# Optimization experiments

Hardware: AMD Instinct MI355X
Metric: run time of the kernel (lower is better)

Reference implementation:

```python
import jax, jax.numpy as jnp
import numpy as np

NBINS = (128, 64, 32)
LOG2PI = float(np.log(2.0 * np.pi))


def _quadratic_spline_stack(x, genes_oi, local_gene_ix, delta, uh, uw):
    """Stack of piecewise-quadratic (piecewise-linear density) splines on [0,1].
    Per split with n heights / n-1 widths (n-1 bins). Returns (outputs, logabsdet)."""
    uh_oi = uh[genes_oi]  # [G, sum(n)]
    uw_oi = uw[genes_oi]  # [G, sum(n-1)]
    outputs = x
    logabsdet = jnp.zeros_like(x)
    oh = ow = od = 0
    for n in NBINS:
        nh, nw = n, n - 1
        uhs = uh_oi[:, oh:oh + nh]
        uws = uw_oi[:, ow:ow + nw]
        ds = delta[:, od:od + nh]
        oh += nh; ow += nw; od += nh
        # per-gene bin widths / locations
        widths_g = jax.nn.softmax(uws, axis=-1)                     # [G, nw]
        bl = jnp.cumsum(widths_g, axis=-1)
        bl = bl.at[:, -1].set(1.0)
        bin_loc_g = jnp.pad(bl, ((0, 0), (1, 0)))                   # [G, nw+1]
        # gather per cut
        w = widths_g[local_gene_ix]                                 # [N, nw]
        loc = bin_loc_g[local_gene_ix]                              # [N, nw+1]
        # per-cut knot heights: gene baseline + cell/gene delta, normalized to unit area
        h_un = jnp.exp(uhs[local_gene_ix] + ds)                     # [N, nh]
        area = jnp.sum(0.5 * (h_un[:, :-1] + h_un[:, 1:]) * w, axis=-1, keepdims=True)
        h = h_un / area                                             # [N, nh]
        seg = 0.5 * (h[:, :-1] + h[:, 1:]) * w                      # bin masses [N, nw]
        left_cdf = jnp.pad(jnp.cumsum(seg, axis=-1)[:, :-1], ((0, 0), (1, 0)))  # [N, nw]
        # locate bin
        bin_idx = jnp.clip(jnp.sum(outputs[:, None] >= loc, axis=-1) - 1, 0, nw - 1)
        gi = bin_idx[:, None]
        loc_l = jnp.take_along_axis(loc, gi, -1)[:, 0]
        w_b = jnp.take_along_axis(w, gi, -1)[:, 0]
        cdf_l = jnp.take_along_axis(left_cdf, gi, -1)[:, 0]
        h_l = jnp.take_along_axis(h, gi, -1)[:, 0]
        h_r = jnp.take_along_axis(h, gi + 1, -1)[:, 0]
        alpha = (outputs - loc_l) / w_b
        outputs = (0.5 * (h_r - h_l) * w_b) * alpha * alpha + h_l * w_b * alpha + cdf_l
        logabsdet = logabsdet + jnp.log(h_l + (h_r - h_l) * alpha)
    return outputs, logabsdet


def setup_inputs() -> dict:
    key = jax.random.key(0)
    ks = jax.random.split(key, 10)
    B, L, G_total, G_oi, C, N = 512, 16, 20000, 500, 224, 200000
    clustering = jax.random.uniform(ks[0], (B, L), dtype=jnp.float32)
    coordinates = jax.random.uniform(ks[1], (N,), dtype=jnp.float32, minval=1e-4, maxval=1.0 - 1e-4)
    genes_oi = jax.random.randint(ks[2], (G_oi,), 0, G_total)
    local_gene_ix = jax.random.randint(ks[3], (N,), 0, G_oi)
    local_cellxgene_ix = jax.random.randint(ks[4], (N,), 0, B * G_oi)
    localcellxgene_ix = jax.random.randint(ks[5], (N,), 0, B * G_total)
    logit_weight = jax.random.normal(ks[6], (G_total, L, C), dtype=jnp.float32) * 0.01
    rho_weight = jax.random.normal(ks[7], (G_total, L), dtype=jnp.float32) * 0.05
    rho_bias = 1e-5 + (1.0 - 1e-5) * jax.random.uniform(ks[8], (G_total,), dtype=jnp.float32)
    k9, k10 = jax.random.split(ks[9])
    unnormalized_heights = jax.random.normal(k9, (G_total, sum(NBINS)), dtype=jnp.float32) * 0.1
    unnormalized_widths = jax.random.normal(k10, (G_total, sum(n - 1 for n in NBINS)), dtype=jnp.float32) * 0.1
    return dict(clustering=clustering, coordinates=coordinates, genes_oi=genes_oi,
                local_gene_ix=local_gene_ix, local_cellxgene_ix=local_cellxgene_ix,
                localcellxgene_ix=localcellxgene_ix, logit_weight=logit_weight,
                rho_weight=rho_weight, rho_bias=rho_bias,
                unnormalized_heights=unnormalized_heights,
                unnormalized_widths=unnormalized_widths)


def reference(clustering, coordinates, genes_oi, local_gene_ix, local_cellxgene_ix,
              localcellxgene_ix, logit_weight, rho_weight, rho_bias,
              unnormalized_heights, unnormalized_widths):
    B = clustering.shape[0]
    G = genes_oi.shape[0]
    n_total_genes = rho_bias.shape[0]
    # Decoder (n_layers=0 -> nn_output = latent)
    lw_oi = logit_weight[genes_oi]                                   # [G, L, C]
    mixture_delta = jnp.einsum('bl,glc->bgc', clustering, lw_oi)     # [B, G, C]
    rho_delta = clustering @ rho_weight.T                            # [B, G_total]
    rho = jax.nn.softmax(jnp.log(rho_bias)[None, :] + rho_delta, axis=-1)
    rho_cuts = rho.reshape(-1)[localcellxgene_ix]                    # [N]
    md_cuts = mixture_delta.reshape(B * G, -1)[local_cellxgene_ix]   # [N, C]
    _, lik_mixture = _quadratic_spline_stack(coordinates, genes_oi, local_gene_ix,
                                             md_cuts, unnormalized_heights, unnormalized_widths)
    lik_overall = jnp.log(rho_cuts) + jnp.log(jnp.float32(n_total_genes))
    elbo = -jnp.sum(lik_mixture + lik_overall)
    # Normal(0, exp(log_scale=0)=1) regularization log-probs
    def normal_logpdf(v):
        return -0.5 * v * v - 0.5 * LOG2PI
    elbo = elbo - jnp.sum(normal_logpdf(lw_oi))
    elbo = elbo - jnp.sum(normal_logpdf(rho_weight[genes_oi]))
    return elbo
```

## Files before the change

kernel.cpp:

```cpp
#include <hip/hip_runtime.h>
#include <cstddef>

#define LOG2PI_F 1.8378770664093453f

typedef float f2 __attribute__((ext_vector_type(2)));

__device__ __forceinline__ float wave_sum(float v) {
#pragma unroll
    for (int o = 32; o >= 1; o >>= 1) v += __shfl_xor(v, o, 64);
    return v;
}
__device__ __forceinline__ float wave_max(float v) {
#pragma unroll
    for (int o = 32; o >= 1; o >>= 1) v = fmaxf(v, __shfl_xor(v, o, 64));
    return v;
}
__device__ __forceinline__ float wave_scan_incl(float v, int lane) {
#pragma unroll
    for (int o = 1; o < 64; o <<= 1) {
        float t = __shfl_up(v, o, 64);
        if (lane >= o) v += t;
    }
    return v;
}

__device__ __forceinline__ float dot16(const f2* __restrict__ a, const f2* __restrict__ b) {
    f2 dv = a[0] * b[0];
#pragma unroll
    for (int l = 1; l < 8; ++l) dv = __builtin_elementwise_fma(a[l], b[l], dv);
    return dv.x + dv.y;
}

__global__ void k_prep_genes(const int* __restrict__ genes_oi,
                             const float* __restrict__ uh, const float* __restrict__ uw,
                             float4* __restrict__ pk, int* __restrict__ counts, int G_oi) {
    const int g = blockIdx.x;
    const int t = threadIdx.x;
    if (t == 0) counts[g] = 0;
    const int gs = genes_oi[g];
    const float* uhg = uh + (size_t)gs * 224;
    const float* uwg = uw + (size_t)gs * 221;

    const int NH[3] = {128, 64, 32};
    const int OH[3] = {0, 128, 192};
    const int OW[3] = {0, 127, 190};
    const int SO[3] = {0, 128, 191};
#pragma unroll
    for (int lev = 0; lev < 3; ++lev) {
        const int nw = NH[lev] - 1;
        float v0 = (t < nw)      ? uwg[OW[lev] + t]      : -INFINITY;
        float v1 = (t + 64 < nw) ? uwg[OW[lev] + t + 64] : -INFINITY;
        float mx = wave_max(fmaxf(v0, v1));
        float e0 = (t < nw)      ? __expf(v0 - mx) : 0.f;
        float e1 = (t + 64 < nw) ? __expf(v1 - mx) : 0.f;
        float inv = 1.0f / wave_sum(e0 + e1);
        float w0 = e0 * inv, w1 = e1 * inv;
        float i0 = wave_scan_incl(w0, t);
        float tot0 = __shfl(i0, 63, 64);
        float i1 = wave_scan_incl(w1, t) + tot0;
        if (t < nw) {
            float loc = (t == nw - 1) ? 1.0f : i0;
            pk[(size_t)(SO[lev] + t) * G_oi + g] = make_float4(uhg[OH[lev] + t + 1], 0.5f * w0, loc, 0.f);
        }
        if (t + 64 < nw) {
            int j = t + 64;
            float loc = (j == nw - 1) ? 1.0f : i1;
            pk[(size_t)(SO[lev] + j) * G_oi + g] = make_float4(uhg[OH[lev] + j + 1], 0.5f * w1, loc, 0.f);
        }
    }
    if (t == 0) pk[(size_t)127 * G_oi + g] = make_float4(uhg[0], uhg[128], uhg[192], 0.f);
}

__global__ void k_prep_lwT(const int* __restrict__ genes_oi,
                           const float* __restrict__ lw, const float* __restrict__ rw,
                           float* __restrict__ lwT, float* __restrict__ pB) {
    const int g = blockIdx.x;
    const int tid = threadIdx.x;
    const int gs = genes_oi[g];
    const float* src = lw + (size_t)gs * 3584;
    float* dst = lwT + (size_t)g * 3584;
    float acc = 0.f;
    if (tid < 224) {
        float vv[16];
#pragma unroll
        for (int l = 0; l < 16; ++l) {
            float v = src[l * 224 + tid];
            vv[l] = v;
            acc = fmaf(v, v, acc);
        }
        float4* d4 = (float4*)(dst + (size_t)tid * 16);
#pragma unroll
        for (int q = 0; q < 4; ++q)
            d4[q] = make_float4(vv[4 * q + 0], vv[4 * q + 1], vv[4 * q + 2], vv[4 * q + 3]);
    }
    if (tid < 16) { float v = rw[(size_t)gs * 16 + tid]; acc = fmaf(v, v, acc); }
    __shared__ float sm[256];
    sm[tid] = acc;
    __syncthreads();
    for (int o = 128; o > 0; o >>= 1) { if (tid < o) sm[tid] += sm[tid + o]; __syncthreads(); }
    if (tid == 0) pB[g] = 0.5f * sm[0] + 0.5f * LOG2PI_F * (3584.0f + 16.0f);
}

__global__ void k_hist_logrb(const int* __restrict__ lcx, int* __restrict__ counts,
                             const float* __restrict__ rho_bias, float* __restrict__ logrb,
                             int N, int G_oi, int G_total) {
    int i = blockIdx.x * blockDim.x + threadIdx.x;
    if (i < G_total) logrb[i] = __logf(rho_bias[i]);
    if (i < N) atomicAdd(&counts[(unsigned)lcx[i] % (unsigned)G_oi], 1);
}

__global__ void k_scan(const int* __restrict__ counts, int* __restrict__ offsets,
                       int* __restrict__ cursor, int G_oi) {
    __shared__ int sm[512];
    const int t = threadIdx.x;
    int v = (t < G_oi) ? counts[t] : 0;
    sm[t] = v;
    __syncthreads();
    for (int o = 1; o < 512; o <<= 1) {
        int add = (t >= o) ? sm[t - o] : 0;
        __syncthreads();
        sm[t] += add;
        __syncthreads();
    }
    if (t < G_oi) {
        offsets[t + 1] = sm[t];
        cursor[t] = sm[t] - v;
    }
    if (t == 0) offsets[0] = 0;
}

__global__ void k_scatter(const float* __restrict__ coord, const int* __restrict__ lgix,
                          const int* __restrict__ lcx, const int* __restrict__ lc2,
                          int* __restrict__ cursor, float4* __restrict__ xv, int N, int G_oi) {
    int i = blockIdx.x * blockDim.x + threadIdx.x;
    if (i >= N) return;
    unsigned v = (unsigned)lcx[i];
    unsigned g = v % (unsigned)G_oi;
    int pos = atomicAdd(&cursor[g], 1);
    int b1 = (int)(v / (unsigned)G_oi);
    xv[pos] = make_float4(coord[i], __int_as_float((b1 << 16) | lgix[i]),
                          __int_as_float(lc2[i]), 0.f);
}

__global__ void k_lse4(const float* __restrict__ clustering, const float* __restrict__ rw,
                       const float* __restrict__ logrb, float* __restrict__ lse,
                       int G_total, int B) {
    const int b0 = blockIdx.x * 4;
    const int tid = threadIdx.x;
    const int nc = min(4, B - b0);

    f2 cl[4][8];
#pragma unroll
    for (int c = 0; c < 4; ++c) {
        if (c < nc) {
            const float4* c4 = (const float4*)(clustering + (size_t)(b0 + c) * 16);
#pragma unroll
            for (int q = 0; q < 4; ++q) {
                float4 v = c4[q];
                cl[c][2 * q + 0] = (f2){v.x, v.y};
                cl[c][2 * q + 1] = (f2){v.z, v.w};
            }
        } else {
#pragma unroll
            for (int l = 0; l < 8; ++l) cl[c][l] = (f2){0.f, 0.f};
        }
    }

    float m[4], s[4];
#pragma unroll
    for (int c = 0; c < 4; ++c) { m[c] = -INFINITY; s[c] = 0.f; }

    for (int g = tid; g < G_total; g += 256) {
        const float4* r4 = (const float4*)(rw + (size_t)g * 16);
        f2 rv[8];
#pragma unroll
        for (int q = 0; q < 4; ++q) {
            float4 v = r4[q];
            rv[2 * q + 0] = (f2){v.x, v.y};
            rv[2 * q + 1] = (f2){v.z, v.w};
        }
        const float lb = logrb[g];
#pragma unroll
        for (int c = 0; c < 4; ++c) {
            float d = dot16(cl[c], rv);
            float logit = lb + d;
            float mn = fmaxf(m[c], logit);
            s[c] = s[c] * __expf(m[c] - mn) + __expf(logit - mn);
            m[c] = mn;
        }
    }

    __shared__ float ms[4][256], ss[4][256];
#pragma unroll
    for (int c = 0; c < 4; ++c) { ms[c][tid] = m[c]; ss[c][tid] = s[c]; }
    __syncthreads();
    for (int o = 128; o > 0; o >>= 1) {
        if (tid < o) {
#pragma unroll
            for (int c = 0; c < 4; ++c) {
                float m2 = ms[c][tid + o], s2 = ss[c][tid + o];
                float mn = fmaxf(ms[c][tid], m2);
                ss[c][tid] = ss[c][tid] * __expf(ms[c][tid] - mn) + s2 * __expf(m2 - mn);
                ms[c][tid] = mn;
            }
        }
        __syncthreads();
    }
    if (tid < 4 && tid < nc) lse[b0 + tid] = ms[tid][0] + __logf(ss[tid][0]);
}

__launch_bounds__(512, 4)
__global__ void k_main2(const float4* __restrict__ xv,
                        const int* __restrict__ offsets,
                        const float* __restrict__ clustering,
                        const float* __restrict__ lwT,
                        const float4* __restrict__ pk,
                        const float* __restrict__ rw,
                        const float* __restrict__ logrb,
                        const float* __restrict__ lse,
                        float* __restrict__ pA, int G_oi, int G_total) {
    const int g = blockIdx.x;
    const int tid = threadIdx.x;
    const float* lwg = lwT + (size_t)g * 3584;
    const int s = offsets[g], e = offsets[g + 1];
    const float logGt = __logf((float)G_total);
    float acc = 0.f;

    __shared__ int    s_cnt[512];
    __shared__ int    s_cur[512];
    __shared__ float4 s_v[512];
    __shared__ float  wsm[8];

    for (int base = s; base < e; base += 512) {
        const int cnt = min(512, e - base);
        const bool valid = tid < cnt;
        float4 v0 = xv[valid ? base + tid : s];
        const int gh_0 = __float_as_int(v0.y) & 0xffff;

        s_cnt[tid] = 0;
        __syncthreads();
        if (valid) atomicAdd(&s_cnt[gh_0], 1);
        __syncthreads();
        int v = s_cnt[tid];
        for (int o = 1; o < 512; o <<= 1) {
            int add = (tid >= o) ? s_cnt[tid - o] : 0;
            __syncthreads();
            s_cnt[tid] += add;
            __syncthreads();
        }
        s_cur[tid] = s_cnt[tid] - v;
        __syncthreads();
        if (valid) {
            int pos = atomicAdd(&s_cur[gh_0], 1);
            s_v[pos] = v0;
        }
        __syncthreads();

        if (valid) {
            float4 vv = s_v[tid];
            float x = vv.x;
            const int meta = __float_as_int(vv.y);
            const int gh  = meta & 0xffff;
            const int b1  = meta >> 16;
            const int lc2 = __float_as_int(vv.z);

            f2 cl[8];
            {
                const float4* c4 = (const float4*)(clustering + (size_t)b1 * 16);
#pragma unroll
                for (int q = 0; q < 4; ++q) {
                    float4 t4 = c4[q];
                    cl[2 * q + 0] = (f2){t4.x, t4.y};
                    cl[2 * q + 1] = (f2){t4.z, t4.w};
                }
            }
            const float4 uh0 = pk[(size_t)127 * G_oi + gh];
            const float uh0v[3] = {uh0.x, uh0.y, uh0.z};

            float lad = 0.f;
            const int NH[3] = {128, 64, 32};
            const int OH[3] = {0, 128, 192};
            const int SO[3] = {0, 128, 191};
#pragma unroll
            for (int lev = 0; lev < 3; ++lev) {
                const int nw = NH[lev] - 1;
                const float* rowbase = lwg + (size_t)OH[lev] * 16;
                float hp = __expf(uh0v[lev] + dot16((const f2*)rowbase, cl));
                float h_l = hp, h_r = hp, whb = 0.f, loc_l = 0.f, cdf = 0.f, area = 0.f;
                int in = 0;
                const float4* pks = pk + (size_t)SO[lev] * G_oi + gh;
                for (int j = 0; j < nw; ++j) {
                    const f2* row = (const f2*)(rowbase + (size_t)(j + 1) * 16);
                    float d = dot16(row, cl);
                    float4 pkv = *pks;
                    pks += G_oi;
                    float hn = __expf(pkv.x + d);
                    float seg = (hp + hn) * pkv.y;
                    bool inJ = (in == j);
                    if (inJ) { h_r = hn; whb = pkv.y; }
                    bool adv = (x >= pkv.z) && (j < nw - 1);
                    if (adv) { cdf += seg; h_l = hn; loc_l = pkv.z; in = j + 1; }
                    area += seg;
                    hp = hn;
                }
                float inv_area = __builtin_amdgcn_rcpf(area);
                float alpha = (x - loc_l) * 0.5f * __builtin_amdgcn_rcpf(whb);
                float t2 = whb * alpha;
                x = (t2 * fmaf(h_r - h_l, alpha, 2.f * h_l) + cdf) * inv_area;
                lad += __logf(fmaf(h_r - h_l, alpha, h_l)) - __logf(area);
            }

            unsigned b2 = (unsigned)lc2 / (unsigned)G_total;
            unsigned gt = (unsigned)lc2 - b2 * (unsigned)G_total;
            f2 c2[8], r2[8];
            {
                const float4* c24 = (const float4*)(clustering + (size_t)b2 * 16);
                const float4* r4  = (const float4*)(rw + (size_t)gt * 16);
#pragma unroll
                for (int q = 0; q < 4; ++q) {
                    float4 a = c24[q], b = r4[q];
                    c2[2 * q + 0] = (f2){a.x, a.y}; c2[2 * q + 1] = (f2){a.z, a.w};
                    r2[2 * q + 0] = (f2){b.x, b.y}; r2[2 * q + 1] = (f2){b.z, b.w};
                }
            }
            float d2 = dot16(c2, r2);
            float lik = logrb[gt] + d2 - lse[b2] + logGt;
            acc -= (lad + lik);
        }
    }

    acc = wave_sum(acc);
    if ((tid & 63) == 0) wsm[tid >> 6] = acc;
    __syncthreads();
    if (tid == 0) {
        float t = 0.f;
#pragma unroll
        for (int w = 0; w < 8; ++w) t += wsm[w];
        pA[g] = t;
    }
}

__global__ void k_final(const float* __restrict__ pA, const float* __restrict__ pB,
                        float* __restrict__ out, int nA, int nB) {
    const int tid = threadIdx.x;
    float acc = 0.f;
    for (int i = tid; i < nA; i += blockDim.x) acc += pA[i];
    for (int i = tid; i < nB; i += blockDim.x) acc += pB[i];
    __shared__ float sm[256];
    sm[tid] = acc;
    __syncthreads();
    for (int o = 128; o > 0; o >>= 1) { if (tid < o) sm[tid] += sm[tid + o]; __syncthreads(); }
    if (tid == 0) out[0] = sm[0];
}

extern "C" void kernel_launch(void* const* d_in, const int* in_sizes, int n_in,
                              void* d_out, int out_size, void* d_ws, size_t ws_size,
                              hipStream_t stream) {
    const float* clustering        = (const float*)d_in[0];
    const float* coordinates       = (const float*)d_in[1];
    const int*   genes_oi          = (const int*)d_in[2];
    const int*   local_gene_ix     = (const int*)d_in[3];
    const int*   local_cellxgene_ix= (const int*)d_in[4];
    const int*   localcellxgene_ix = (const int*)d_in[5];
    const float* lw                = (const float*)d_in[6];
    const float* rw                = (const float*)d_in[7];
    const float* rho_bias          = (const float*)d_in[8];
    const float* uh                = (const float*)d_in[9];
    const float* uw                = (const float*)d_in[10];

    const int G_total = in_sizes[8];
    const int G_oi    = in_sizes[2];
    const int N       = in_sizes[1];
    const int L       = in_sizes[7] / G_total;
    const int B       = in_sizes[0] / L;

    size_t off = 0;
    char* base = (char*)d_ws;
    auto alloc = [&](size_t nbytes) {
        char* p = base + off;
        off = (off + nbytes + 15) & ~(size_t)15;
        return (void*)p;
    };
    float*  pA      = (float*)alloc(sizeof(float) * (G_oi + 16));
    float*  pB      = (float*)alloc(sizeof(float) * (G_oi + 16));
    float*  lse     = (float*)alloc(sizeof(float) * (B + 16));
    float*  logrb   = (float*)alloc(sizeof(float) * G_total);
    float*  lwT     = (float*)alloc(sizeof(float) * (size_t)G_oi * 3584);
    float4* pk      = (float4*)alloc(sizeof(float4) * (size_t)G_oi * 224);
    int*    counts  = (int*)alloc(sizeof(int) * 512);
    int*    offsets = (int*)alloc(sizeof(int) * 512);
    int*    cursor  = (int*)alloc(sizeof(int) * 512);
    float4* xv      = (float4*)alloc(sizeof(float4) * (size_t)N);
    (void)ws_size;

    const int TPB = 256;
    k_prep_genes<<<G_oi, 64, 0, stream>>>(genes_oi, uh, uw, pk, counts, G_oi);
    k_prep_lwT<<<G_oi, 256, 0, stream>>>(genes_oi, lw, rw, lwT, pB);
    k_hist_logrb<<<(N + TPB - 1) / TPB, TPB, 0, stream>>>(local_cellxgene_ix, counts,
                                                          rho_bias, logrb, N, G_oi, G_total);
    k_scan<<<1, 512, 0, stream>>>(counts, offsets, cursor, G_oi);
    k_scatter<<<(N + TPB - 1) / TPB, TPB, 0, stream>>>(coordinates, local_gene_ix,
                                                       local_cellxgene_ix, localcellxgene_ix,
                                                       cursor, xv, N, G_oi);
    k_lse4<<<(B + 3) / 4, 256, 0, stream>>>(clustering, rw, logrb, lse, G_total, B);
    k_main2<<<G_oi, 512, 0, stream>>>(xv, offsets, clustering, lwT, pk,
                                      rw, logrb, lse, pA, G_oi, G_total);
    k_final<<<1, 256, 0, stream>>>(pA, pB, (float*)d_out, G_oi, G_oi);
}
```

Before: 633.4 us.

## Precompute per-cluster-gene mixture deltas and bucket cuts by local gene

Adds a kernel that computes the mixture delta (clustering × logit weights) once for every (cluster, gene, knot) into a dense table D. The main kernel then reads a precomputed row per cut, so it no longer does a 16-wide dot product for every knot of every cut. Cuts are now bucketed by local gene index instead of by cellxgene modulo, and each block keeps its gene's spline parameters in shared memory; the in-block regrouping sort is removed. The lse kernel is retuned to 2 clusters per block, and the trade-off is extra workspace and memory traffic to write and read D.

```diff
diff --git a/kernel.cpp b/kernel.cpp
--- a/kernel.cpp
+++ b/kernel.cpp
@@ -33,13 +33,14 @@
 
 __global__ void k_prep_genes(const int* __restrict__ genes_oi,
                              const float* __restrict__ uh, const float* __restrict__ uw,
-                             float4* __restrict__ pk, int* __restrict__ counts, int G_oi) {
+                             float4* __restrict__ pk, int* __restrict__ counts) {
     const int g = blockIdx.x;
     const int t = threadIdx.x;
     if (t == 0) counts[g] = 0;
     const int gs = genes_oi[g];
     const float* uhg = uh + (size_t)gs * 224;
     const float* uwg = uw + (size_t)gs * 221;
+    float4* pkg = pk + (size_t)g * 224;
 
     const int NH[3] = {128, 64, 32};
     const int OH[3] = {0, 128, 192};
@@ -60,15 +61,15 @@
         float i1 = wave_scan_incl(w1, t) + tot0;
         if (t < nw) {
             float loc = (t == nw - 1) ? 1.0f : i0;
-            pk[(size_t)(SO[lev] + t) * G_oi + g] = make_float4(uhg[OH[lev] + t + 1], 0.5f * w0, loc, 0.f);
+            pkg[SO[lev] + t] = make_float4(uhg[OH[lev] + t + 1], 0.5f * w0, loc, 0.f);
         }
         if (t + 64 < nw) {
             int j = t + 64;
             float loc = (j == nw - 1) ? 1.0f : i1;
-            pk[(size_t)(SO[lev] + j) * G_oi + g] = make_float4(uhg[OH[lev] + j + 1], 0.5f * w1, loc, 0.f);
-        }
-    }
-    if (t == 0) pk[(size_t)127 * G_oi + g] = make_float4(uhg[0], uhg[128], uhg[192], 0.f);
+            pkg[SO[lev] + j] = make_float4(uhg[OH[lev] + j + 1], 0.5f * w1, loc, 0.f);
+        }
+    }
+    if (t == 0) pkg[127] = make_float4(uhg[0], uhg[128], uhg[192], 0.f);
 }
 
 __global__ void k_prep_lwT(const int* __restrict__ genes_oi,
@@ -101,12 +102,36 @@
     if (tid == 0) pB[g] = 0.5f * sm[0] + 0.5f * LOG2PI_F * (3584.0f + 16.0f);
 }
 
-__global__ void k_hist_logrb(const int* __restrict__ lcx, int* __restrict__ counts,
+__launch_bounds__(256)
+__global__ void k_mixd(const float* __restrict__ clustering,
+                       const float* __restrict__ lwT,
+                       float* __restrict__ D, int G_oi, int B) {
+    const int g = blockIdx.x;
+    const int j = threadIdx.x;
+    __shared__ float cls[8192];
+    for (int i = threadIdx.x; i < B * 16; i += 256) cls[i] = clustering[i];
+    __syncthreads();
+    if (j >= 224) return;
+    f2 lwr[8];
+    const float4* src = (const float4*)(lwT + ((size_t)g * 224 + j) * 16);
+#pragma unroll
+    for (int q = 0; q < 4; ++q) {
+        float4 v = src[q];
+        lwr[2 * q + 0] = (f2){v.x, v.y};
+        lwr[2 * q + 1] = (f2){v.z, v.w};
+    }
+    for (int b = 0; b < B; ++b) {
+        const f2* cb = (const f2*)(cls + b * 16);
+        D[((size_t)b * G_oi + g) * 224 + j] = dot16(lwr, cb);
+    }
+}
+
+__global__ void k_hist_logrb(const int* __restrict__ lgix, int* __restrict__ counts,
                              const float* __restrict__ rho_bias, float* __restrict__ logrb,
-                             int N, int G_oi, int G_total) {
+                             int N, int G_total) {
     int i = blockIdx.x * blockDim.x + threadIdx.x;
     if (i < G_total) logrb[i] = __logf(rho_bias[i]);
-    if (i < N) atomicAdd(&counts[(unsigned)lcx[i] % (unsigned)G_oi], 1);
+    if (i < N) atomicAdd(&counts[lgix[i]], 1);
 }
 
 __global__ void k_scan(const int* __restrict__ counts, int* __restrict__ offsets,
@@ -131,27 +156,23 @@
 
 __global__ void k_scatter(const float* __restrict__ coord, const int* __restrict__ lgix,
                           const int* __restrict__ lcx, const int* __restrict__ lc2,
-                          int* __restrict__ cursor, float4* __restrict__ xv, int N, int G_oi) {
+                          int* __restrict__ cursor, float4* __restrict__ xv, int N) {
     int i = blockIdx.x * blockDim.x + threadIdx.x;
     if (i >= N) return;
-    unsigned v = (unsigned)lcx[i];
-    unsigned g = v % (unsigned)G_oi;
-    int pos = atomicAdd(&cursor[g], 1);
-    int b1 = (int)(v / (unsigned)G_oi);
-    xv[pos] = make_float4(coord[i], __int_as_float((b1 << 16) | lgix[i]),
-                          __int_as_float(lc2[i]), 0.f);
-}
-
-__global__ void k_lse4(const float* __restrict__ clustering, const float* __restrict__ rw,
+    int pos = atomicAdd(&cursor[lgix[i]], 1);
+    xv[pos] = make_float4(coord[i], __int_as_float(lcx[i]), __int_as_float(lc2[i]), 0.f);
+}
+
+__global__ void k_lse2(const float* __restrict__ clustering, const float* __restrict__ rw,
                        const float* __restrict__ logrb, float* __restrict__ lse,
                        int G_total, int B) {
-    const int b0 = blockIdx.x * 4;
+    const int b0 = blockIdx.x * 2;
     const int tid = threadIdx.x;
-    const int nc = min(4, B - b0);
-
-    f2 cl[4][8];
-#pragma unroll
-    for (int c = 0; c < 4; ++c) {
+    const int nc = min(2, B - b0);
+
+    f2 cl[2][8];
+#pragma unroll
+    for (int c = 0; c < 2; ++c) {
         if (c < nc) {
             const float4* c4 = (const float4*)(clustering + (size_t)(b0 + c) * 16);
 #pragma unroll
@@ -166,9 +187,9 @@
         }
     }
 
-    float m[4], s[4];
-#pragma unroll
-    for (int c = 0; c < 4; ++c) { m[c] = -INFINITY; s[c] = 0.f; }
+    float m[2], s[2];
+#pragma unroll
+    for (int c = 0; c < 2; ++c) { m[c] = -INFINITY; s[c] = 0.f; }
 
     for (int g = tid; g < G_total; g += 256) {
         const float4* r4 = (const float4*)(rw + (size_t)g * 16);
@@ -181,7 +202,7 @@
         }
         const float lb = logrb[g];
 #pragma unroll
-        for (int c = 0; c < 4; ++c) {
+        for (int c = 0; c < 2; ++c) {
             float d = dot16(cl[c], rv);
             float logit = lb + d;
             float mn = fmaxf(m[c], logit);
@@ -190,14 +211,14 @@
         }
     }
 
-    __shared__ float ms[4][256], ss[4][256];
-#pragma unroll
-    for (int c = 0; c < 4; ++c) { ms[c][tid] = m[c]; ss[c][tid] = s[c]; }
+    __shared__ float ms[2][256], ss[2][256];
+#pragma unroll
+    for (int c = 0; c < 2; ++c) { ms[c][tid] = m[c]; ss[c][tid] = s[c]; }
     __syncthreads();
     for (int o = 128; o > 0; o >>= 1) {
         if (tid < o) {
 #pragma unroll
-            for (int c = 0; c < 4; ++c) {
+            for (int c = 0; c < 2; ++c) {
                 float m2 = ms[c][tid + o], s2 = ss[c][tid + o];
                 float mn = fmaxf(ms[c][tid], m2);
                 ss[c][tid] = ss[c][tid] * __expf(ms[c][tid] - mn) + s2 * __expf(m2 - mn);
@@ -206,76 +227,39 @@
         }
         __syncthreads();
     }
-    if (tid < 4 && tid < nc) lse[b0 + tid] = ms[tid][0] + __logf(ss[tid][0]);
+    if (tid < 2 && tid < nc) lse[b0 + tid] = ms[tid][0] + __logf(ss[tid][0]);
 }
 
 __launch_bounds__(512, 4)
-__global__ void k_main2(const float4* __restrict__ xv,
+__global__ void k_main3(const float4* __restrict__ xv,
                         const int* __restrict__ offsets,
                         const float* __restrict__ clustering,
-                        const float* __restrict__ lwT,
                         const float4* __restrict__ pk,
+                        const float* __restrict__ D,
                         const float* __restrict__ rw,
                         const float* __restrict__ logrb,
                         const float* __restrict__ lse,
                         float* __restrict__ pA, int G_oi, int G_total) {
     const int g = blockIdx.x;
     const int tid = threadIdx.x;
-    const float* lwg = lwT + (size_t)g * 3584;
+    __shared__ float4 s_pk[224];
+    __shared__ float wsm[8];
+    if (tid < 224) s_pk[tid] = pk[(size_t)g * 224 + tid];
+    __syncthreads();
+
     const int s = offsets[g], e = offsets[g + 1];
     const float logGt = __logf((float)G_total);
+    const float4 uh0 = s_pk[127];
     float acc = 0.f;
 
-    __shared__ int    s_cnt[512];
-    __shared__ int    s_cur[512];
-    __shared__ float4 s_v[512];
-    __shared__ float  wsm[8];
-
     for (int base = s; base < e; base += 512) {
-        const int cnt = min(512, e - base);
-        const bool valid = tid < cnt;
-        float4 v0 = xv[valid ? base + tid : s];
-        const int gh_0 = __float_as_int(v0.y) & 0xffff;
-
-        s_cnt[tid] = 0;
-        __syncthreads();
-        if (valid) atomicAdd(&s_cnt[gh_0], 1);
-        __syncthreads();
-        int v = s_cnt[tid];
-        for (int o = 1; o < 512; o <<= 1) {
-            int add = (tid >= o) ? s_cnt[tid - o] : 0;
-            __syncthreads();
-            s_cnt[tid] += add;
-            __syncthreads();
-        }
-        s_cur[tid] = s_cnt[tid] - v;
-        __syncthreads();
-        if (valid) {
-            int pos = atomicAdd(&s_cur[gh_0], 1);
-            s_v[pos] = v0;
-        }
-        __syncthreads();
-
-        if (valid) {
-            float4 vv = s_v[tid];
+        const int i = base + tid;
+        if (i < e) {
+            float4 vv = xv[i];
             float x = vv.x;
-            const int meta = __float_as_int(vv.y);
-            const int gh  = meta & 0xffff;
-            const int b1  = meta >> 16;
+            const int lcx = __float_as_int(vv.y);
             const int lc2 = __float_as_int(vv.z);
-
-            f2 cl[8];
-            {
-                const float4* c4 = (const float4*)(clustering + (size_t)b1 * 16);
-#pragma unroll
-                for (int q = 0; q < 4; ++q) {
-                    float4 t4 = c4[q];
-                    cl[2 * q + 0] = (f2){t4.x, t4.y};
-                    cl[2 * q + 1] = (f2){t4.z, t4.w};
-                }
-            }
-            const float4 uh0 = pk[(size_t)127 * G_oi + gh];
-            const float uh0v[3] = {uh0.x, uh0.y, uh0.z};
+            const float* Drow = D + (size_t)lcx * 224;
 
             float lad = 0.f;
             const int NH[3] = {128, 64, 32};
@@ -283,26 +267,40 @@
             const int SO[3] = {0, 128, 191};
 #pragma unroll
             for (int lev = 0; lev < 3; ++lev) {
-                const int nw = NH[lev] - 1;
-                const float* rowbase = lwg + (size_t)OH[lev] * 16;
-                float hp = __expf(uh0v[lev] + dot16((const f2*)rowbase, cl));
+                const int nh = NH[lev];
+                const float* dbase = Drow + OH[lev];
+                const float uh0l = (lev == 0) ? uh0.x : ((lev == 1) ? uh0.y : uh0.z);
+                const float4* spk = s_pk + SO[lev];
+
+                float4 dq = *(const float4*)(dbase);
+                float hp = __expf(uh0l + dq.x);
                 float h_l = hp, h_r = hp, whb = 0.f, loc_l = 0.f, cdf = 0.f, area = 0.f;
                 int in = 0;
-                const float4* pks = pk + (size_t)SO[lev] * G_oi + gh;
-                for (int j = 0; j < nw; ++j) {
-                    const f2* row = (const f2*)(rowbase + (size_t)(j + 1) * 16);
-                    float d = dot16(row, cl);
-                    float4 pkv = *pks;
-                    pks += G_oi;
-                    float hn = __expf(pkv.x + d);
+
+                auto STEP = [&](int j, float dval, bool last) {
+                    float4 pkv = spk[j];
+                    float hn = __expf(pkv.x + dval);
                     float seg = (hp + hn) * pkv.y;
-                    bool inJ = (in == j);
-                    if (inJ) { h_r = hn; whb = pkv.y; }
-                    bool adv = (x >= pkv.z) && (j < nw - 1);
+                    if (in == j) { h_r = hn; whb = pkv.y; }
+                    bool adv = (x >= pkv.z) && !last;
                     if (adv) { cdf += seg; h_l = hn; loc_l = pkv.z; in = j + 1; }
                     area += seg;
                     hp = hn;
+                };
+
+                STEP(0, dq.y, false);
+                STEP(1, dq.z, false);
+                STEP(2, dq.w, false);
+                const int nq = nh / 4;
+                for (int q = 1; q < nq; ++q) {
+                    dq = *(const float4*)(dbase + 4 * q);
+                    const bool lastq = (q == nq - 1);
+                    STEP(4 * q - 1, dq.x, false);
+                    STEP(4 * q + 0, dq.y, false);
+                    STEP(4 * q + 1, dq.z, false);
+                    STEP(4 * q + 2, dq.w, lastq);
                 }
+
                 float inv_area = __builtin_amdgcn_rcpf(area);
                 float alpha = (x - loc_l) * 0.5f * __builtin_amdgcn_rcpf(whb);
                 float t2 = whb * alpha;
@@ -391,19 +389,21 @@
     int*    offsets = (int*)alloc(sizeof(int) * 512);
     int*    cursor  = (int*)alloc(sizeof(int) * 512);
     float4* xv      = (float4*)alloc(sizeof(float4) * (size_t)N);
+    float*  D       = (float*)alloc(sizeof(float) * (size_t)B * G_oi * 224);
     (void)ws_size;
 
     const int TPB = 256;
-    k_prep_genes<<<G_oi, 64, 0, stream>>>(genes_oi, uh, uw, pk, counts, G_oi);
+    k_prep_genes<<<G_oi, 64, 0, stream>>>(genes_oi, uh, uw, pk, counts);
     k_prep_lwT<<<G_oi, 256, 0, stream>>>(genes_oi, lw, rw, lwT, pB);
-    k_hist_logrb<<<(N + TPB - 1) / TPB, TPB, 0, stream>>>(local_cellxgene_ix, counts,
-                                                          rho_bias, logrb, N, G_oi, G_total);
+    k_mixd<<<G_oi, 256, 0, stream>>>(clustering, lwT, D, G_oi, B);
+    k_hist_logrb<<<(N + TPB - 1) / TPB, TPB, 0, stream>>>(local_gene_ix, counts,
+                                                          rho_bias, logrb, N, G_total);
     k_scan<<<1, 512, 0, stream>>>(counts, offsets, cursor, G_oi);
     k_scatter<<<(N + TPB - 1) / TPB, TPB, 0, stream>>>(coordinates, local_gene_ix,
                                                        local_cellxgene_ix, localcellxgene_ix,
-                                                       cursor, xv, N, G_oi);
-    k_lse4<<<(B + 3) / 4, 256, 0, stream>>>(clustering, rw, logrb, lse, G_total, B);
-    k_main2<<<G_oi, 512, 0, stream>>>(xv, offsets, clustering, lwT, pk,
+                                                       cursor, xv, N);
+    k_lse2<<<(B + 1) / 2, 256, 0, stream>>>(clustering, rw, logrb, lse, G_total, B);
+    k_main3<<<G_oi, 512, 0, stream>>>(xv, offsets, clustering, pk, D,
                                       rw, logrb, lse, pA, G_oi, G_total);
     k_final<<<1, 256, 0, stream>>>(pA, pB, (float*)d_out, G_oi, G_oi);
 }
```

New measurement: 931.0 us. +47.0%, slower.
